# Optimization experiments

Hardware: AMD Instinct MI355X
Metric: run time of the kernel (lower is better)

Reference implementation:

```python
import jax, jax.numpy as jnp
import numpy as np

M, Q, H, L = 1, 9, 512, 2

def lstm_seq(x, w_ih, w_hh, b, reverse=False):
    # x: [B, T, Din] -> outputs [B, T, H], final (h, c) each [B, H]
    B = x.shape[0]
    h0 = jnp.zeros((B, H), x.dtype)
    xw = jnp.einsum('btd,gd->btg', x, w_ih) + b  # [B, T, 4H] input projection, precomputed
    def step(carry, xt):
        h, c = carry
        g = xt + h @ w_hh.T
        i, f, gg, o = jnp.split(g, 4, axis=-1)  # torch gate order: i, f, g, o
        c = jax.nn.sigmoid(f) * c + jax.nn.sigmoid(i) * jnp.tanh(gg)
        h = jax.nn.sigmoid(o) * jnp.tanh(c)
        return (h, c), h
    (hT, cT), hs = jax.lax.scan(step, (h0, h0), jnp.swapaxes(xw, 0, 1), reverse=reverse)
    return jnp.swapaxes(hs, 0, 1), hT, cT

def _forward(X, future_features, Y_teacher,
             enc_w_ih_l0, enc_w_hh_l0, enc_b_l0, enc_w_ih_l0r, enc_w_hh_l0r, enc_b_l0r,
             enc_w_ih_l1, enc_w_hh_l1, enc_b_l1, enc_w_ih_l1r, enc_w_hh_l1r, enc_b_l1r,
             dec_w_ih_l0, dec_w_hh_l0, dec_b_l0, dec_w_ih_l1, dec_w_hh_l1, dec_b_l1,
             bidi_w_h, bidi_b_h, out_w, out_b, horizon_span):
    B = X.shape[0]
    enc = [((enc_w_ih_l0, enc_w_hh_l0, enc_b_l0), (enc_w_ih_l0r, enc_w_hh_l0r, enc_b_l0r)),
           ((enc_w_ih_l1, enc_w_hh_l1, enc_b_l1), (enc_w_ih_l1r, enc_w_hh_l1r, enc_b_l1r))]
    inp, hs, cs = X, [], []
    for fw, bw in enc:  # bidirectional multilayer encoder
        of, hf, cf = lstm_seq(inp, *fw, reverse=False)
        ob, hb, cb = lstm_seq(inp, *bw, reverse=True)
        inp = jnp.concatenate([of, ob], axis=-1)
        hs += [hf, hb]; cs += [cf, cb]
    h = jnp.stack(hs)  # [2L, B, H], torch order (l0_fwd, l0_bwd, l1_fwd, l1_bwd)
    c = jnp.stack(cs)
    def merge(s):  # NOTE: original applies bidi_project__h / nonlin__h to BOTH h and c
        s = s.reshape(L, 2, B, H)
        s = jnp.concatenate([s[:, 0], s[:, 1]], axis=2)       # [L, B, 2H]
        s = jnp.swapaxes(s, 0, 1).reshape(B, 2 * L * H)
        s = jax.nn.elu(s @ bidi_w_h.T + bidi_b_h)             # [B, L*H]
        return jnp.swapaxes(s.reshape(B, L, H), 0, 1)         # [L, B, H]
    h, c = merge(h), merge(c)
    dec = [(dec_w_ih_l0, dec_w_hh_l0, dec_b_l0), (dec_w_ih_l1, dec_w_hh_l1, dec_b_l1)]
    def dec_step(carry, f_t):
        h, c, y_prev = carry
        x = jnp.concatenate([y_prev, f_t], axis=-1)  # [B, M + d_future_features]
        nh, nc = [], []
        for l, (w_ih, w_hh, b) in enumerate(dec):
            g = x @ w_ih.T + h[l] @ w_hh.T + b
            i, f, gg, o = jnp.split(g, 4, axis=-1)
            cl = jax.nn.sigmoid(f) * c[l] + jax.nn.sigmoid(i) * jnp.tanh(gg)
            x = jax.nn.sigmoid(o) * jnp.tanh(cl)
            nh.append(x); nc.append(cl)
        y = x @ out_w.T + out_b                       # [B, M*Q]
        return (jnp.stack(nh), jnp.stack(nc), y[:, :M]), y
    y0 = X[:, -1, :M]
    _, ys = jax.lax.scan(dec_step, (h, c, y0), jnp.swapaxes(future_features, 0, 1))
    T = future_features.shape[1]
    return jnp.swapaxes(ys, 0, 1).reshape(B, T, M, Q)

def setup_inputs() -> dict:
    key = jax.random.key(0)
    ks = iter(jax.random.split(key, 40))
    s = 0.05
    d = {
        'X': jax.random.normal(next(ks), (64, 256, 9), jnp.float32),
        'future_features': jax.random.normal(next(ks), (64, 96, 8), jnp.float32),
        'Y_teacher': jax.random.normal(next(ks), (64, 96, 1), jnp.float32),
    }
    shapes = {
        'enc_w_ih_l0': (2048, 9), 'enc_w_hh_l0': (2048, 512), 'enc_b_l0': (2048,),
        'enc_w_ih_l0r': (2048, 9), 'enc_w_hh_l0r': (2048, 512), 'enc_b_l0r': (2048,),
        'enc_w_ih_l1': (2048, 1024), 'enc_w_hh_l1': (2048, 512), 'enc_b_l1': (2048,),
        'enc_w_ih_l1r': (2048, 1024), 'enc_w_hh_l1r': (2048, 512), 'enc_b_l1r': (2048,),
        'dec_w_ih_l0': (2048, 9), 'dec_w_hh_l0': (2048, 512), 'dec_b_l0': (2048,),
        'dec_w_ih_l1': (2048, 512), 'dec_w_hh_l1': (2048, 512), 'dec_b_l1': (2048,),
        'bidi_w_h': (1024, 2048), 'bidi_b_h': (1024,),
        'out_w': (9, 512), 'out_b': (9,),
    }
    for name, shp in shapes.items():
        d[name] = jax.random.normal(next(ks), shp, jnp.float32) * s
    d['horizon_span'] = 96
    return d

def reference(X, future_features, Y_teacher,
              enc_w_ih_l0, enc_w_hh_l0, enc_b_l0, enc_w_ih_l0r, enc_w_hh_l0r, enc_b_l0r,
              enc_w_ih_l1, enc_w_hh_l1, enc_b_l1, enc_w_ih_l1r, enc_w_hh_l1r, enc_b_l1r,
              dec_w_ih_l0, dec_w_hh_l0, dec_b_l0, dec_w_ih_l1, dec_w_hh_l1, dec_b_l1,
              bidi_w_h, bidi_b_h, out_w, out_b, horizon_span):
    return _forward(X, future_features, Y_teacher,
                    enc_w_ih_l0, enc_w_hh_l0, enc_b_l0, enc_w_ih_l0r, enc_w_hh_l0r, enc_b_l0r,
                    enc_w_ih_l1, enc_w_hh_l1, enc_b_l1, enc_w_ih_l1r, enc_w_hh_l1r, enc_b_l1r,
                    dec_w_ih_l0, dec_w_hh_l0, dec_b_l0, dec_w_ih_l1, dec_w_hh_l1, dec_b_l1,
                    bidi_w_h, bidi_b_h, out_w, out_b, horizon_span)
```

## Files before the change

### kernel.cpp

```cpp
#include <hip/hip_runtime.h>


#define BLOCKS 256

typedef short bf16x8 __attribute__((ext_vector_type(8)));
typedef float f32x4  __attribute__((ext_vector_type(4)));
typedef unsigned short u16;

__device__ __forceinline__ f32x4 MFMA16(bf16x8 a, bf16x8 b, f32x4 c) {
  return __builtin_amdgcn_mfma_f32_16x16x32_bf16(a, b, c, 0, 0, 0);
}

__device__ __forceinline__ u16 bfr(float f) {
  unsigned u = __float_as_uint(f);
  u += 0x7FFFu + ((u >> 16) & 1u);
  return (u16)(u >> 16);
}
__device__ __forceinline__ bf16x8 pack8(float4 a, float4 b) {
  bf16x8 r;
  r[0] = (short)bfr(a.x); r[1] = (short)bfr(a.y); r[2] = (short)bfr(a.z); r[3] = (short)bfr(a.w);
  r[4] = (short)bfr(b.x); r[5] = (short)bfr(b.y); r[6] = (short)bfr(b.z); r[7] = (short)bfr(b.w);
  return r;
}
__device__ __forceinline__ bf16x8 loadW8(const float* p) {
  float4 a = *(const float4*)p;
  float4 b = *(const float4*)(p + 4);
  return pack8(a, b);
}
__device__ __forceinline__ float sigm(float x) { return 1.0f / (1.0f + __expf(-x)); }
__device__ __forceinline__ float tanh_f(float x) {
  float a = fabsf(x);
  float e = __expf(-2.0f * a);
  float t = (1.0f - e) / (1.0f + e);
  return x < 0.0f ? -t : t;
}
__device__ __forceinline__ float lstm_h(const float pre[4], float& c) {
  float ig = sigm(pre[0]);
  float fg = sigm(pre[1]);
  float gg = tanh_f(pre[2]);
  float og = sigm(pre[3]);
  c = fg * c + ig * gg;
  return og * tanh_f(c);
}

__device__ __forceinline__ void st_b16_coh(u16* p, u16 v) {
  unsigned uv = v;
  asm volatile("global_store_short %0, %1, off sc0 sc1" :: "v"(p), "v"(uv) : "memory");
}
__device__ __forceinline__ void st_f32_coh(float* p, float v) {
  asm volatile("global_store_dword %0, %1, off sc0 sc1" :: "v"(p), "v"(v) : "memory");
}
__device__ __forceinline__ void st_u32_coh(unsigned* p, unsigned v) {
  asm volatile("global_store_dword %0, %1, off sc0 sc1" :: "v"(p), "v"(v) : "memory");
}
__device__ __forceinline__ float ld_f32_coh(const float* p) {
  float r;
  asm volatile("global_load_dword %0, %1, off sc0 sc1\n\ts_waitcnt vmcnt(0)"
               : "=&v"(r) : "v"(p) : "memory");
  return r;
}
__device__ __forceinline__ unsigned ld_u32_coh(const unsigned* p) {
  unsigned r;
  asm volatile("global_load_dword %0, %1, off sc0 sc1\n\ts_waitcnt vmcnt(0)"
               : "=&v"(r) : "v"(p) : "memory");
  return r;
}
__device__ __forceinline__ void ld_tile_coh(const u16* base, bf16x8 f[16]) {
  asm volatile(
    "global_load_dwordx4 %0, %16, off sc0 sc1\n\t"
    "global_load_dwordx4 %1, %16, off offset:64 sc0 sc1\n\t"
    "global_load_dwordx4 %2, %16, off offset:128 sc0 sc1\n\t"
    "global_load_dwordx4 %3, %16, off offset:192 sc0 sc1\n\t"
    "global_load_dwordx4 %4, %16, off offset:256 sc0 sc1\n\t"
    "global_load_dwordx4 %5, %16, off offset:320 sc0 sc1\n\t"
    "global_load_dwordx4 %6, %16, off offset:384 sc0 sc1\n\t"
    "global_load_dwordx4 %7, %16, off offset:448 sc0 sc1\n\t"
    "global_load_dwordx4 %8, %16, off offset:512 sc0 sc1\n\t"
    "global_load_dwordx4 %9, %16, off offset:576 sc0 sc1\n\t"
    "global_load_dwordx4 %10, %16, off offset:640 sc0 sc1\n\t"
    "global_load_dwordx4 %11, %16, off offset:704 sc0 sc1\n\t"
    "global_load_dwordx4 %12, %16, off offset:768 sc0 sc1\n\t"
    "global_load_dwordx4 %13, %16, off offset:832 sc0 sc1\n\t"
    "global_load_dwordx4 %14, %16, off offset:896 sc0 sc1\n\t"
    "global_load_dwordx4 %15, %16, off offset:960 sc0 sc1\n\t"
    "s_waitcnt vmcnt(0)"
    : "=&v"(f[0]), "=&v"(f[1]), "=&v"(f[2]), "=&v"(f[3]),
      "=&v"(f[4]), "=&v"(f[5]), "=&v"(f[6]), "=&v"(f[7]),
      "=&v"(f[8]), "=&v"(f[9]), "=&v"(f[10]), "=&v"(f[11]),
      "=&v"(f[12]), "=&v"(f[13]), "=&v"(f[14]), "=&v"(f[15])
    : "v"(base)
    : "memory");
}

static constexpr size_t OFF_GO   = 32768;
static constexpr size_t OFF_YF   = 32896;
static constexpr size_t SZ_SLOT  = (size_t)64 * 512 * 2;
static constexpr size_t OFF_OF   = 65536;
static constexpr size_t OFF_OBR  = OFF_OF  + 257 * SZ_SLOT;
static constexpr size_t OFF_H1F  = OFF_OBR + 257 * SZ_SLOT;
static constexpr size_t OFF_H1B  = OFF_H1F + 2 * SZ_SLOT;
static constexpr size_t OFF_DH0  = OFF_H1B + 2 * SZ_SLOT;
static constexpr size_t OFF_DH1  = OFF_DH0 + 2 * SZ_SLOT;
static constexpr size_t OFF_SBUF = OFF_DH1 + 2 * SZ_SLOT;
static constexpr size_t OFF_CDEC = OFF_SBUF + (size_t)128 * 2048 * 4;
static constexpr size_t OFF_Y    = OFF_CDEC + (size_t)2 * 64 * 512 * 4;
static constexpr size_t WS_NEED  = OFF_Y + 256;

__device__ __forceinline__ void gridbar(char* ws, unsigned e) {
  asm volatile("s_waitcnt vmcnt(0)" ::: "memory");
  __syncthreads();
  unsigned* flags = (unsigned*)ws;
  unsigned* go    = (unsigned*)(ws + OFF_GO);
  const int tid = threadIdx.x;
  if (blockIdx.x == 0) {
    if (tid != 0) {
      const unsigned* fp = flags + (size_t)tid * 32;
      while (ld_u32_coh(fp) < e) {}
    }
    __syncthreads();
    if (tid == 0) st_u32_coh(go, e);
  } else {
    if (tid == 0) {
      st_u32_coh(flags + (size_t)blockIdx.x * 32, e);
      while (ld_u32_coh(go) < e) { __builtin_amdgcn_s_sleep(1); }
    }
    __syncthreads();
  }
}

__global__ __launch_bounds__(256, 1) void red_lstm(
    const float* __restrict__ X,   const float* __restrict__ FUT,
    const float* __restrict__ eWih0,  const float* __restrict__ eWhh0,  const float* __restrict__ eB0,
    const float* __restrict__ eWih0r, const float* __restrict__ eWhh0r, const float* __restrict__ eB0r,
    const float* __restrict__ eWih1,  const float* __restrict__ eWhh1,  const float* __restrict__ eB1,
    const float* __restrict__ eWih1r, const float* __restrict__ eWhh1r, const float* __restrict__ eB1r,
    const float* __restrict__ dWih0,  const float* __restrict__ dWhh0,  const float* __restrict__ dB0,
    const float* __restrict__ dWih1,  const float* __restrict__ dWhh1,  const float* __restrict__ dB1,
    const float* __restrict__ bW,  const float* __restrict__ bB,
    const float* __restrict__ oW,  const float* __restrict__ oB,
    float* __restrict__ OUT, char* __restrict__ ws)
{
  const int blk  = blockIdx.x;
  const int tid  = threadIdx.x;
  const int lane = tid & 63;
  const int wave = tid >> 6;
  const int n16  = lane & 15;
  const int quad = lane >> 4;
  const int rowg = wave * 16 + n16;
  const int jl   = tid & 3;
  const int bb   = tid >> 2;

  u16*   OF  = (u16*)(ws + OFF_OF);
  u16*   OBR = (u16*)(ws + OFF_OBR);
  u16*   H1F = (u16*)(ws + OFF_H1F);
  u16*   H1B = (u16*)(ws + OFF_H1B);
  u16*   DH0 = (u16*)(ws + OFF_DH0);
  u16*   DH1 = (u16*)(ws + OFF_DH1);
  float* SB  = (float*)(ws + OFF_SBUF);
  float* CD  = (float*)(ws + OFF_CDEC);
  float* YB  = (float*)(ws + OFF_Y);
  unsigned* YFLAG = (unsigned*)(ws + OFF_YF);

  __shared__ float g_s[64 * 20];
  unsigned ep = 0;

  {
    const bool fw = (blk < 128);
    const int  hb = fw ? blk : (blk - 128);
    const int  j0 = hb * 4;
    const int  col = j0 + (n16 & 3) + 512 * (n16 >> 2);
    const float* whh = fw ? eWhh0 : eWhh0r;
    const float* wih = fw ? eWih0 : eWih0r;
    const float* bia = fw ? eB0 : eB0r;
    u16* buf = fw ? OF : OBR;

    bf16x8 B[16];
    {
      const float* wr = whh + (size_t)col * 512 + quad * 8;
      #pragma unroll
      for (int kk = 0; kk < 16; ++kk) B[kk] = loadW8(wr + kk * 32);
    }
    float wr9[4][9], b4[4];
    #pragma unroll
    for (int g = 0; g < 4; ++g) {
      int cg = j0 + jl + 512 * g;
      b4[g] = bia[cg];
      #pragma unroll
      for (int k = 0; k < 9; ++k) wr9[g][k] = wih[cg * 9 + k];
    }
    float c = 0.0f;

    #pragma unroll 1
    for (int s = 0; s < 256; ++s) {
      bf16x8 T[16];
      ld_tile_coh(buf + ((size_t)s * 64 + rowg) * 512 + quad * 8, T);
      f32x4 a0 = {0.f,0.f,0.f,0.f}, a1 = {0.f,0.f,0.f,0.f};
      #pragma unroll
      for (int kk = 0; kk < 16; kk += 2) {
        a0 = MFMA16(T[kk],     B[kk],     a0);
        a1 = MFMA16(T[kk + 1], B[kk + 1], a1);
      }
      f32x4 acc = a0 + a1;
      #pragma unroll
      for (int r = 0; r < 4; ++r)
        g_s[(wave * 16 + quad * 4 + r) * 20 + n16] = acc[r];
      __syncthreads();

      const int t = fw ? s : (255 - s);
      float pre[4];
      #pragma unroll
      for (int g = 0; g < 4; ++g) pre[g] = g_s[bb * 20 + jl + 4 * g] + b4[g];
      const float* xp = X + ((size_t)bb * 256 + t) * 9;
      #pragma unroll
      for (int k = 0; k < 9; ++k) {
        float xv = xp[k];
        #pragma unroll
        for (int g = 0; g < 4; ++g) pre[g] += xv * wr9[g][k];
      }
      float h = lstm_h(pre, c);
      st_b16_coh(buf + ((size_t)(s + 1) * 64 + bb) * 512 + j0 + jl, bfr(h));
      if (s == 255) {
        int co = fw ? 0 : 512;
        st_f32_coh(SB + (size_t)bb * 2048 + co + j0 + jl, h);
        st_f32_coh(SB + (size_t)(64 + bb) * 2048 + co + j0 + jl, c);
      }
      gridbar(ws, ++ep);
    }
  }

  {
    const bool fw = (blk < 128);
    const int  hb = fw ? blk : (blk - 128);
    const int  j0 = hb * 4;
    const int  col = j0 + (n16 & 3) + 512 * (n16 >> 2);
    const float* whh = fw ? eWhh1 : eWhh1r;
    const float* wih = fw ? eWih1 : eWih1r;
    const float* bia = fw ? eB1 : eB1r;
    u16* hpp = fw ? H1F : H1B;

    bf16x8 B[48];
    {
      const float* wr = whh + (size_t)col * 512 + quad * 8;
      #pragma unroll
      for (int kk = 0; kk < 16; ++kk) B[kk] = loadW8(wr + kk * 32);
      const float* wr2 = wih + (size_t)col * 1024 + quad * 8;
      #pragma unroll
      for (int kk = 0; kk < 32; ++kk) B[16 + kk] = loadW8(wr2 + kk * 32);
    }
    float b4[4];
    #pragma unroll
    for (int g = 0; g < 4; ++g) b4[g] = bia[j0 + jl + 512 * g];
    float c = 0.0f;

    #pragma unroll 1
    for (int s = 0; s < 256; ++s) {
      const int slot_of = fw ? (s + 1)   : (256 - s);
      const int slot_ob = fw ? (256 - s) : (s + 1);
      f32x4 a0 = {0.f,0.f,0.f,0.f}, a1 = {0.f,0.f,0.f,0.f};
      {
        bf16x8 T[16];
        ld_tile_coh(hpp + ((size_t)(s & 1) * 64 + rowg) * 512 + quad * 8, T);
        #pragma unroll
        for (int kk = 0; kk < 16; kk += 2) {
          a0 = MFMA16(T[kk],     B[kk],     a0);
          a1 = MFMA16(T[kk + 1], B[kk + 1], a1);
        }
      }
      {
        bf16x8 T[16];
        ld_tile_coh(OF + ((size_t)slot_of * 64 + rowg) * 512 + quad * 8, T);
        #pragma unroll
        for (int kk = 0; kk < 16; kk += 2) {
          a0 = MFMA16(T[kk],     B[16 + kk],     a0);
          a1 = MFMA16(T[kk + 1], B[16 + kk + 1], a1);
        }
      }
      {
        bf16x8 T[16];
        ld_tile_coh(OBR + ((size_t)slot_ob * 64 + rowg) * 512 + quad * 8, T);
        #pragma unroll
        for (int kk = 0; kk < 16; kk += 2) {
          a0 = MFMA16(T[kk],     B[32 + kk],     a0);
          a1 = MFMA16(T[kk + 1], B[32 + kk + 1], a1);
        }
      }
      f32x4 acc = a0 + a1;
      #pragma unroll
      for (int r = 0; r < 4; ++r)
        g_s[(wave * 16 + quad * 4 + r) * 20 + n16] = acc[r];
      __syncthreads();

      float pre[4];
      #pragma unroll
      for (int g = 0; g < 4; ++g) pre[g] = g_s[bb * 20 + jl + 4 * g] + b4[g];
      float h = lstm_h(pre, c);
      st_b16_coh(hpp + ((size_t)((s & 1) ^ 1) * 64 + bb) * 512 + j0 + jl, bfr(h));
      if (s == 255) {
        int co = fw ? 1024 : 1536;
        st_f32_coh(SB + (size_t)bb * 2048 + co + j0 + jl, h);
        st_f32_coh(SB + (size_t)(64 + bb) * 2048 + co + j0 + jl, c);
      }
      gridbar(ws, ++ep);
    }
  }

  {
    if (blk < 128) {
      const int colm = blk * 8 + (tid & 7);
      const int rg   = tid >> 3;
      const float* wrow = bW + (size_t)colm * 2048;
      float am[4];
      #pragma unroll
      for (int r = 0; r < 4; ++r) am[r] = bB[colm];
      #pragma unroll 1
      for (int k = 0; k < 2048; k += 4) {
        float4 w = *(const float4*)(wrow + k);
        #pragma unroll
        for (int r = 0; r < 4; ++r) {
          float4 a = *(const float4*)(SB + (size_t)(rg * 4 + r) * 2048 + k);
          am[r] += a.x * w.x + a.y * w.y + a.z * w.z + a.w * w.w;
        }
      }
      const int l = colm >> 9, j = colm & 511;
      #pragma unroll
      for (int r = 0; r < 4; ++r) {
        int row = rg * 4 + r;
        float v = am[r];
        v = v > 0.f ? v : (__expf(v) - 1.0f);
        if (row < 64) {
          u16* dst = l ? DH1 : DH0;
          st_b16_coh(dst + (size_t)row * 512 + j, bfr(v));
        } else {
          st_f32_coh(CD + ((size_t)l * 64 + (row - 64)) * 512 + j, v);
        }
      }
    }
    gridbar(ws, ++ep);
  }

  {
    const bool isL0 = (blk < 128);
    const int  hb = isL0 ? blk : (blk - 128);
    const int  j0 = hb * 4;
    const int  col = j0 + (n16 & 3) + 512 * (n16 >> 2);

    bf16x8 BD[32];
    float wr9[4][9], b4[4], c;
    if (isL0) {
      const float* wr = dWhh0 + (size_t)col * 512 + quad * 8;
      #pragma unroll
      for (int kk = 0; kk < 16; ++kk) BD[kk] = loadW8(wr + kk * 32);
      #pragma unroll
      for (int g = 0; g < 4; ++g) {
        int cg = j0 + jl + 512 * g;
        b4[g] = dB0[cg];
        #pragma unroll
        for (int k = 0; k < 9; ++k) wr9[g][k] = dWih0[cg * 9 + k];
      }
      c = CD[(size_t)bb * 512 + j0 + jl];
    } else {
      const float* wr = dWhh1 + (size_t)col * 512 + quad * 8;
      #pragma unroll
      for (int kk = 0; kk < 16; ++kk) BD[kk] = loadW8(wr + kk * 32);
      const float* wr2 = dWih1 + (size_t)col * 512 + quad * 8;
      #pragma unroll
      for (int kk = 0; kk < 16; ++kk) BD[16 + kk] = loadW8(wr2 + kk * 32);
      #pragma unroll
      for (int g = 0; g < 4; ++g) b4[g] = dB1[j0 + jl + 512 * g];
      c = CD[((size_t)64 + bb) * 512 + j0 + jl];
    }
    bf16x8 OBW[16];
    float obv = 0.0f;
    if (blk == 128) {
      if (n16 < 9) {
        const float* wr = oW + (size_t)n16 * 512 + quad * 8;
        #pragma unroll
        for (int kk = 0; kk < 16; ++kk) OBW[kk] = loadW8(wr + kk * 32);
        obv = oB[n16];
      } else {
        #pragma unroll
        for (int kk = 0; kk < 16; ++kk) {
          bf16x8 z = {0,0,0,0,0,0,0,0};
          OBW[kk] = z;
        }
      }
    }

    #pragma unroll 1
    for (int t = 0; t < 96; ++t) {
      if (blk == 128 && t >= 1) {
        bf16x8 T[16];
        ld_tile_coh(DH1 + ((size_t)(t & 1) * 64 + rowg) * 512 + quad * 8, T);
        f32x4 a0 = {0.f,0.f,0.f,0.f}, a1 = {0.f,0.f,0.f,0.f};
        #pragma unroll
        for (int kk = 0; kk < 16; kk += 2) {
          a0 = MFMA16(T[kk],     OBW[kk],     a0);
          a1 = MFMA16(T[kk + 1], OBW[kk + 1], a1);
        }
        f32x4 acc = a0 + a1;
        #pragma unroll
        for (int r = 0; r < 4; ++r) {
          int b = wave * 16 + quad * 4 + r;
          float v = acc[r] + obv;
          if (n16 < 9) {
            OUT[(size_t)b * 864 + (size_t)(t - 1) * 9 + n16] = v;
            if (n16 == 0) st_f32_coh(YB + b, v);
          }
        }
        asm volatile("s_waitcnt vmcnt(0)" ::: "memory");
        __syncthreads();
        if (tid == 0) st_u32_coh(YFLAG, (unsigned)t);
      }
      if (isL0) {
        bf16x8 T[16];
        ld_tile_coh(DH0 + ((size_t)(t & 1) * 64 + rowg) * 512 + quad * 8, T);
        f32x4 a0 = {0.f,0.f,0.f,0.f}, a1 = {0.f,0.f,0.f,0.f};
        #pragma unroll
        for (int kk = 0; kk < 16; kk += 2) {
          a0 = MFMA16(T[kk],     BD[kk],     a0);
          a1 = MFMA16(T[kk + 1], BD[kk + 1], a1);
        }
        f32x4 acc = a0 + a1;
        #pragma unroll
        for (int r = 0; r < 4; ++r)
          g_s[(wave * 16 + quad * 4 + r) * 20 + n16] = acc[r];
        __syncthreads();
        if (t >= 1 && tid == 0) {
          while (ld_u32_coh(YFLAG) < (unsigned)t) {}
        }
        __syncthreads();
        float pre[4];
        #pragma unroll
        for (int g = 0; g < 4; ++g) pre[g] = g_s[bb * 20 + jl + 4 * g] + b4[g];
        float yp = (t == 0) ? X[((size_t)bb * 256 + 255) * 9] : ld_f32_coh(YB + bb);
        #pragma unroll
        for (int g = 0; g < 4; ++g) pre[g] += yp * wr9[g][0];
        const float* fp = FUT + ((size_t)bb * 96 + t) * 8;
        #pragma unroll
        for (int k = 0; k < 8; ++k) {
          float fv = fp[k];
          #pragma unroll
          for (int g = 0; g < 4; ++g) pre[g] += fv * wr9[g][k + 1];
        }
        float h = lstm_h(pre, c);
        st_b16_coh(DH0 + ((size_t)((t & 1) ^ 1) * 64 + bb) * 512 + j0 + jl, bfr(h));
      }
      gridbar(ws, ++ep);

      if (!isL0) {
        f32x4 a0 = {0.f,0.f,0.f,0.f}, a1 = {0.f,0.f,0.f,0.f};
        {
          bf16x8 T[16];
          ld_tile_coh(DH1 + ((size_t)(t & 1) * 64 + rowg) * 512 + quad * 8, T);
          #pragma unroll
          for (int kk = 0; kk < 16; kk += 2) {
            a0 = MFMA16(T[kk],     BD[kk],     a0);
            a1 = MFMA16(T[kk + 1], BD[kk + 1], a1);
          }
        }
        {
          bf16x8 T[16];
          ld_tile_coh(DH0 + ((size_t)((t & 1) ^ 1) * 64 + rowg) * 512 + quad * 8, T);
          #pragma unroll
          for (int kk = 0; kk < 16; kk += 2) {
            a0 = MFMA16(T[kk],     BD[16 + kk],     a0);
            a1 = MFMA16(T[kk + 1], BD[16 + kk + 1], a1);
          }
        }
        f32x4 acc = a0 + a1;
        #pragma unroll
        for (int r = 0; r < 4; ++r)
          g_s[(wave * 16 + quad * 4 + r) * 20 + n16] = acc[r];
        __syncthreads();
        float pre[4];
        #pragma unroll
        for (int g = 0; g < 4; ++g) pre[g] = g_s[bb * 20 + jl + 4 * g] + b4[g];
        float h = lstm_h(pre, c);
        st_b16_coh(DH1 + ((size_t)((t & 1) ^ 1) * 64 + bb) * 512 + j0 + jl, bfr(h));
      }
      gridbar(ws, ++ep);
    }

    if (blk == 128) {
      bf16x8 T[16];
      ld_tile_coh(DH1 + ((size_t)0 * 64 + rowg) * 512 + quad * 8, T);
      f32x4 a0 = {0.f,0.f,0.f,0.f}, a1 = {0.f,0.f,0.f,0.f};
      #pragma unroll
      for (int kk = 0; kk < 16; kk += 2) {
        a0 = MFMA16(T[kk],     OBW[kk],     a0);
        a1 = MFMA16(T[kk + 1], OBW[kk + 1], a1);
      }
      f32x4 acc = a0 + a1;
      #pragma unroll
      for (int r = 0; r < 4; ++r) {
        int b = wave * 16 + quad * 4 + r;
        float v = acc[r] + obv;
        if (n16 < 9) OUT[(size_t)b * 864 + (size_t)95 * 9 + n16] = v;
      }
    }
  }
}

extern "C" void kernel_launch(void* const* d_in, const int* in_sizes, int n_in,
                              void* d_out, int out_size, void* d_ws, size_t ws_size,
                              hipStream_t stream) {
  (void)in_sizes; (void)n_in; (void)out_size;
  if (ws_size < WS_NEED) return;

  const float* X      = (const float*)d_in[0];
  const float* FUT    = (const float*)d_in[1];
  const float* eWih0  = (const float*)d_in[3];
  const float* eWhh0  = (const float*)d_in[4];
  const float* eB0    = (const float*)d_in[5];
  const float* eWih0r = (const float*)d_in[6];
  const float* eWhh0r = (const float*)d_in[7];
  const float* eB0r   = (const float*)d_in[8];
  const float* eWih1  = (const float*)d_in[9];
  const float* eWhh1  = (const float*)d_in[10];
  const float* eB1    = (const float*)d_in[11];
  const float* eWih1r = (const float*)d_in[12];
  const float* eWhh1r = (const float*)d_in[13];
  const float* eB1r   = (const float*)d_in[14];
  const float* dWih0  = (const float*)d_in[15];
  const float* dWhh0  = (const float*)d_in[16];
  const float* dB0    = (const float*)d_in[17];
  const float* dWih1  = (const float*)d_in[18];
  const float* dWhh1  = (const float*)d_in[19];
  const float* dB1    = (const float*)d_in[20];
  const float* bW     = (const float*)d_in[21];
  const float* bB     = (const float*)d_in[22];
  const float* oW     = (const float*)d_in[23];
  const float* oB     = (const float*)d_in[24];

  char* ws = (char*)d_ws;
  hipMemsetAsync(ws, 0, 65536, stream);
  hipMemsetAsync(ws + OFF_OF, 0, SZ_SLOT, stream);
  hipMemsetAsync(ws + OFF_OBR, 0, SZ_SLOT, stream);
  hipMemsetAsync(ws + OFF_H1F, 0, SZ_SLOT, stream);
  hipMemsetAsync(ws + OFF_H1B, 0, SZ_SLOT, stream);

  red_lstm<<<BLOCKS, 256, 0, stream>>>(
      X, FUT,
      eWih0, eWhh0, eB0, eWih0r, eWhh0r, eB0r,
      eWih1, eWhh1, eB1, eWih1r, eWhh1r, eB1r,
      dWih0, dWhh0, dB0, dWih1, dWhh1, dB1,
      bW, bB, oW, oB,
      (float*)d_out, ws);
}
```

Measured before the change: 4.718 ms.

## Use write-once hidden-state slots with plain cached loads and per-block barrier flags

Hidden-state buffers for every recurrent stage become one slot per timestep instead of ping-pong double buffers. Because each address is now written only once, the A-operand tiles can be read with ordinary cached vector loads interleaved with the MFMAs, instead of coherent inline-asm loads that wait on the whole tile. The grid barrier gives each block its own go flag with no sleep, and the decoder's y feedback is published as per-block records, each with its own flag. This uses much more workspace and relies on stale cache lines never being read for fresh slots, which is a correctness risk if addresses are ever reused.

Result: slower. 6.376 ms (+35.2%).

```diff
diff --git a/kernel.cpp b/kernel.cpp
--- a/kernel.cpp
+++ b/kernel.cpp
@@ -50,14 +50,11 @@
 __device__ __forceinline__ void st_f32_coh(float* p, float v) {
   asm volatile("global_store_dword %0, %1, off sc0 sc1" :: "v"(p), "v"(v) : "memory");
 }
+__device__ __forceinline__ void st_f32x4_coh(float* p, f32x4 v) {
+  asm volatile("global_store_dwordx4 %0, %1, off sc0 sc1" :: "v"(p), "v"(v) : "memory");
+}
 __device__ __forceinline__ void st_u32_coh(unsigned* p, unsigned v) {
   asm volatile("global_store_dword %0, %1, off sc0 sc1" :: "v"(p), "v"(v) : "memory");
-}
-__device__ __forceinline__ float ld_f32_coh(const float* p) {
-  float r;
-  asm volatile("global_load_dword %0, %1, off sc0 sc1\n\ts_waitcnt vmcnt(0)"
-               : "=&v"(r) : "v"(p) : "memory");
-  return r;
 }
 __device__ __forceinline__ unsigned ld_u32_coh(const unsigned* p) {
   unsigned r;
@@ -65,51 +62,28 @@
                : "=&v"(r) : "v"(p) : "memory");
   return r;
 }
-__device__ __forceinline__ void ld_tile_coh(const u16* base, bf16x8 f[16]) {
-  asm volatile(
-    "global_load_dwordx4 %0, %16, off sc0 sc1\n\t"
-    "global_load_dwordx4 %1, %16, off offset:64 sc0 sc1\n\t"
-    "global_load_dwordx4 %2, %16, off offset:128 sc0 sc1\n\t"
-    "global_load_dwordx4 %3, %16, off offset:192 sc0 sc1\n\t"
-    "global_load_dwordx4 %4, %16, off offset:256 sc0 sc1\n\t"
-    "global_load_dwordx4 %5, %16, off offset:320 sc0 sc1\n\t"
-    "global_load_dwordx4 %6, %16, off offset:384 sc0 sc1\n\t"
-    "global_load_dwordx4 %7, %16, off offset:448 sc0 sc1\n\t"
-    "global_load_dwordx4 %8, %16, off offset:512 sc0 sc1\n\t"
-    "global_load_dwordx4 %9, %16, off offset:576 sc0 sc1\n\t"
-    "global_load_dwordx4 %10, %16, off offset:640 sc0 sc1\n\t"
-    "global_load_dwordx4 %11, %16, off offset:704 sc0 sc1\n\t"
-    "global_load_dwordx4 %12, %16, off offset:768 sc0 sc1\n\t"
-    "global_load_dwordx4 %13, %16, off offset:832 sc0 sc1\n\t"
-    "global_load_dwordx4 %14, %16, off offset:896 sc0 sc1\n\t"
-    "global_load_dwordx4 %15, %16, off offset:960 sc0 sc1\n\t"
-    "s_waitcnt vmcnt(0)"
-    : "=&v"(f[0]), "=&v"(f[1]), "=&v"(f[2]), "=&v"(f[3]),
-      "=&v"(f[4]), "=&v"(f[5]), "=&v"(f[6]), "=&v"(f[7]),
-      "=&v"(f[8]), "=&v"(f[9]), "=&v"(f[10]), "=&v"(f[11]),
-      "=&v"(f[12]), "=&v"(f[13]), "=&v"(f[14]), "=&v"(f[15])
-    : "v"(base)
-    : "memory");
-}
-
-static constexpr size_t OFF_GO   = 32768;
-static constexpr size_t OFF_YF   = 32896;
-static constexpr size_t SZ_SLOT  = (size_t)64 * 512 * 2;
-static constexpr size_t OFF_OF   = 65536;
-static constexpr size_t OFF_OBR  = OFF_OF  + 257 * SZ_SLOT;
-static constexpr size_t OFF_H1F  = OFF_OBR + 257 * SZ_SLOT;
-static constexpr size_t OFF_H1B  = OFF_H1F + 2 * SZ_SLOT;
-static constexpr size_t OFF_DH0  = OFF_H1B + 2 * SZ_SLOT;
-static constexpr size_t OFF_DH1  = OFF_DH0 + 2 * SZ_SLOT;
-static constexpr size_t OFF_SBUF = OFF_DH1 + 2 * SZ_SLOT;
-static constexpr size_t OFF_CDEC = OFF_SBUF + (size_t)128 * 2048 * 4;
-static constexpr size_t OFF_Y    = OFF_CDEC + (size_t)2 * 64 * 512 * 4;
-static constexpr size_t WS_NEED  = OFF_Y + 256;
+
+static constexpr size_t OFF_FLAGS = 0;
+static constexpr size_t OFF_GO    = 32768;
+static constexpr size_t SZ_YT     = (size_t)128 * 384;
+static constexpr size_t OFF_YREC  = 65536;
+static constexpr size_t OFF_SB    = OFF_YREC + 96 * SZ_YT;
+static constexpr size_t OFF_CD    = OFF_SB + (size_t)128 * 2048 * 4;
+static constexpr size_t SZ_SLOT   = (size_t)64 * 512 * 2;
+static constexpr size_t OFF_OF    = OFF_CD + (size_t)2 * 64 * 512 * 4;
+static constexpr size_t OFF_OBR   = OFF_OF  + 257 * SZ_SLOT;
+static constexpr size_t OFF_H1F   = OFF_OBR + 257 * SZ_SLOT;
+static constexpr size_t OFF_H1B   = OFF_H1F + 257 * SZ_SLOT;
+static constexpr size_t OFF_DH0   = OFF_H1B + 257 * SZ_SLOT;
+static constexpr size_t OFF_DH1   = OFF_DH0 + 97 * SZ_SLOT;
+static constexpr size_t WS_NEED   = OFF_DH1 + 97 * SZ_SLOT;
+
+#define SLOT_U 32768
 
 __device__ __forceinline__ void gridbar(char* ws, unsigned e) {
   asm volatile("s_waitcnt vmcnt(0)" ::: "memory");
   __syncthreads();
-  unsigned* flags = (unsigned*)ws;
+  unsigned* flags = (unsigned*)(ws + OFF_FLAGS);
   unsigned* go    = (unsigned*)(ws + OFF_GO);
   const int tid = threadIdx.x;
   if (blockIdx.x == 0) {
@@ -118,11 +92,12 @@
       while (ld_u32_coh(fp) < e) {}
     }
     __syncthreads();
-    if (tid == 0) st_u32_coh(go, e);
+    st_u32_coh(go + (size_t)tid * 32, e);
   } else {
     if (tid == 0) {
       st_u32_coh(flags + (size_t)blockIdx.x * 32, e);
-      while (ld_u32_coh(go) < e) { __builtin_amdgcn_s_sleep(1); }
+      const unsigned* gp = go + (size_t)blockIdx.x * 32;
+      while (ld_u32_coh(gp) < e) {}
     }
     __syncthreads();
   }
@@ -156,12 +131,11 @@
   u16*   H1B = (u16*)(ws + OFF_H1B);
   u16*   DH0 = (u16*)(ws + OFF_DH0);
   u16*   DH1 = (u16*)(ws + OFF_DH1);
-  float* SB  = (float*)(ws + OFF_SBUF);
-  float* CD  = (float*)(ws + OFF_CDEC);
-  float* YB  = (float*)(ws + OFF_Y);
-  unsigned* YFLAG = (unsigned*)(ws + OFF_YF);
+  float* SB  = (float*)(ws + OFF_SB);
+  float* CD  = (float*)(ws + OFF_CD);
 
   __shared__ float g_s[64 * 20];
+  __shared__ __align__(16) float y_s[64];
   unsigned ep = 0;
 
   {
@@ -192,13 +166,12 @@
 
     #pragma unroll 1
     for (int s = 0; s < 256; ++s) {
-      bf16x8 T[16];
-      ld_tile_coh(buf + ((size_t)s * 64 + rowg) * 512 + quad * 8, T);
+      const u16* ab = buf + (size_t)s * SLOT_U + rowg * 512 + quad * 8;
       f32x4 a0 = {0.f,0.f,0.f,0.f}, a1 = {0.f,0.f,0.f,0.f};
       #pragma unroll
       for (int kk = 0; kk < 16; kk += 2) {
-        a0 = MFMA16(T[kk],     B[kk],     a0);
-        a1 = MFMA16(T[kk + 1], B[kk + 1], a1);
+        a0 = MFMA16(*(const bf16x8*)(ab + kk * 32),        B[kk],     a0);
+        a1 = MFMA16(*(const bf16x8*)(ab + kk * 32 + 32),   B[kk + 1], a1);
       }
       f32x4 acc = a0 + a1;
       #pragma unroll
@@ -218,7 +191,7 @@
         for (int g = 0; g < 4; ++g) pre[g] += xv * wr9[g][k];
       }
       float h = lstm_h(pre, c);
-      st_b16_coh(buf + ((size_t)(s + 1) * 64 + bb) * 512 + j0 + jl, bfr(h));
+      st_b16_coh(buf + (size_t)(s + 1) * SLOT_U + bb * 512 + j0 + jl, bfr(h));
       if (s == 255) {
         int co = fw ? 0 : 512;
         st_f32_coh(SB + (size_t)bb * 2048 + co + j0 + jl, h);
@@ -256,33 +229,24 @@
     for (int s = 0; s < 256; ++s) {
       const int slot_of = fw ? (s + 1)   : (256 - s);
       const int slot_ob = fw ? (256 - s) : (s + 1);
+      const u16* aH = hpp + (size_t)s * SLOT_U + rowg * 512 + quad * 8;
+      const u16* aF = OF  + (size_t)slot_of * SLOT_U + rowg * 512 + quad * 8;
+      const u16* aB = OBR + (size_t)slot_ob * SLOT_U + rowg * 512 + quad * 8;
       f32x4 a0 = {0.f,0.f,0.f,0.f}, a1 = {0.f,0.f,0.f,0.f};
-      {
-        bf16x8 T[16];
-        ld_tile_coh(hpp + ((size_t)(s & 1) * 64 + rowg) * 512 + quad * 8, T);
-        #pragma unroll
-        for (int kk = 0; kk < 16; kk += 2) {
-          a0 = MFMA16(T[kk],     B[kk],     a0);
-          a1 = MFMA16(T[kk + 1], B[kk + 1], a1);
-        }
-      }
-      {
-        bf16x8 T[16];
-        ld_tile_coh(OF + ((size_t)slot_of * 64 + rowg) * 512 + quad * 8, T);
-        #pragma unroll
-        for (int kk = 0; kk < 16; kk += 2) {
-          a0 = MFMA16(T[kk],     B[16 + kk],     a0);
-          a1 = MFMA16(T[kk + 1], B[16 + kk + 1], a1);
-        }
-      }
-      {
-        bf16x8 T[16];
-        ld_tile_coh(OBR + ((size_t)slot_ob * 64 + rowg) * 512 + quad * 8, T);
-        #pragma unroll
-        for (int kk = 0; kk < 16; kk += 2) {
-          a0 = MFMA16(T[kk],     B[32 + kk],     a0);
-          a1 = MFMA16(T[kk + 1], B[32 + kk + 1], a1);
-        }
+      #pragma unroll
+      for (int kk = 0; kk < 16; kk += 2) {
+        a0 = MFMA16(*(const bf16x8*)(aH + kk * 32),      B[kk],     a0);
+        a1 = MFMA16(*(const bf16x8*)(aH + kk * 32 + 32), B[kk + 1], a1);
+      }
+      #pragma unroll
+      for (int kk = 0; kk < 16; kk += 2) {
+        a0 = MFMA16(*(const bf16x8*)(aF + kk * 32),      B[16 + kk],     a0);
+        a1 = MFMA16(*(const bf16x8*)(aF + kk * 32 + 32), B[16 + kk + 1], a1);
+      }
+      #pragma unroll
+      for (int kk = 0; kk < 16; kk += 2) {
+        a0 = MFMA16(*(const bf16x8*)(aB + kk * 32),      B[32 + kk],     a0);
+        a1 = MFMA16(*(const bf16x8*)(aB + kk * 32 + 32), B[32 + kk + 1], a1);
       }
       f32x4 acc = a0 + a1;
       #pragma unroll
@@ -294,7 +258,7 @@
       #pragma unroll
       for (int g = 0; g < 4; ++g) pre[g] = g_s[bb * 20 + jl + 4 * g] + b4[g];
       float h = lstm_h(pre, c);
-      st_b16_coh(hpp + ((size_t)((s & 1) ^ 1) * 64 + bb) * 512 + j0 + jl, bfr(h));
+      st_b16_coh(hpp + (size_t)(s + 1) * SLOT_U + bb * 512 + j0 + jl, bfr(h));
       if (s == 255) {
         int co = fw ? 1024 : 1536;
         st_f32_coh(SB + (size_t)bb * 2048 + co + j0 + jl, h);
@@ -389,52 +353,55 @@
     #pragma unroll 1
     for (int t = 0; t < 96; ++t) {
       if (blk == 128 && t >= 1) {
-        bf16x8 T[16];
-        ld_tile_coh(DH1 + ((size_t)(t & 1) * 64 + rowg) * 512 + quad * 8, T);
+        const u16* ah = DH1 + (size_t)t * SLOT_U + rowg * 512 + quad * 8;
         f32x4 a0 = {0.f,0.f,0.f,0.f}, a1 = {0.f,0.f,0.f,0.f};
         #pragma unroll
         for (int kk = 0; kk < 16; kk += 2) {
-          a0 = MFMA16(T[kk],     OBW[kk],     a0);
-          a1 = MFMA16(T[kk + 1], OBW[kk + 1], a1);
+          a0 = MFMA16(*(const bf16x8*)(ah + kk * 32),      OBW[kk],     a0);
+          a1 = MFMA16(*(const bf16x8*)(ah + kk * 32 + 32), OBW[kk + 1], a1);
         }
         f32x4 acc = a0 + a1;
         #pragma unroll
         for (int r = 0; r < 4; ++r) {
           int b = wave * 16 + quad * 4 + r;
           float v = acc[r] + obv;
-          if (n16 < 9) {
-            OUT[(size_t)b * 864 + (size_t)(t - 1) * 9 + n16] = v;
-            if (n16 == 0) st_f32_coh(YB + b, v);
+          if (n16 < 9) OUT[(size_t)b * 864 + (size_t)(t - 1) * 9 + n16] = v;
+          if (n16 == 0) y_s[b] = v;
+        }
+        __syncthreads();
+        {
+          char* yt = ws + OFF_YREC + (size_t)t * SZ_YT;
+          const int rec = tid >> 1, half = tid & 1;
+          float* dst = (float*)(yt + (size_t)rec * 384) + half * 32;
+          #pragma unroll
+          for (int i = 0; i < 8; ++i) {
+            f32x4 v = *(const f32x4*)(y_s + half * 32 + i * 4);
+            st_f32x4_coh(dst + i * 4, v);
           }
         }
         asm volatile("s_waitcnt vmcnt(0)" ::: "memory");
         __syncthreads();
-        if (tid == 0) st_u32_coh(YFLAG, (unsigned)t);
+        if (tid < 128) {
+          unsigned* yf = (unsigned*)(ws + OFF_YREC + (size_t)t * SZ_YT + (size_t)tid * 384 + 256);
+          st_u32_coh(yf, (unsigned)t);
+        }
       }
       if (isL0) {
-        bf16x8 T[16];
-        ld_tile_coh(DH0 + ((size_t)(t & 1) * 64 + rowg) * 512 + quad * 8, T);
+        const u16* ah = DH0 + (size_t)t * SLOT_U + rowg * 512 + quad * 8;
         f32x4 a0 = {0.f,0.f,0.f,0.f}, a1 = {0.f,0.f,0.f,0.f};
         #pragma unroll
         for (int kk = 0; kk < 16; kk += 2) {
-          a0 = MFMA16(T[kk],     BD[kk],     a0);
-          a1 = MFMA16(T[kk + 1], BD[kk + 1], a1);
+          a0 = MFMA16(*(const bf16x8*)(ah + kk * 32),      BD[kk],     a0);
+          a1 = MFMA16(*(const bf16x8*)(ah + kk * 32 + 32), BD[kk + 1], a1);
         }
         f32x4 acc = a0 + a1;
         #pragma unroll
         for (int r = 0; r < 4; ++r)
           g_s[(wave * 16 + quad * 4 + r) * 20 + n16] = acc[r];
         __syncthreads();
-        if (t >= 1 && tid == 0) {
-          while (ld_u32_coh(YFLAG) < (unsigned)t) {}
-        }
-        __syncthreads();
         float pre[4];
         #pragma unroll
         for (int g = 0; g < 4; ++g) pre[g] = g_s[bb * 20 + jl + 4 * g] + b4[g];
-        float yp = (t == 0) ? X[((size_t)bb * 256 + 255) * 9] : ld_f32_coh(YB + bb);
-        #pragma unroll
-        for (int g = 0; g < 4; ++g) pre[g] += yp * wr9[g][0];
         const float* fp = FUT + ((size_t)bb * 96 + t) * 8;
         #pragma unroll
         for (int k = 0; k < 8; ++k) {
@@ -442,30 +409,37 @@
           #pragma unroll
           for (int g = 0; g < 4; ++g) pre[g] += fv * wr9[g][k + 1];
         }
+        float yp;
+        if (t == 0) {
+          yp = X[((size_t)bb * 256 + 255) * 9];
+        } else {
+          char* yr = ws + OFF_YREC + (size_t)t * SZ_YT + (size_t)blk * 384;
+          if (tid == 0) {
+            while (ld_u32_coh((unsigned*)(yr + 256)) < (unsigned)t) {}
+          }
+          __syncthreads();
+          yp = ((const float*)yr)[bb];
+        }
+        #pragma unroll
+        for (int g = 0; g < 4; ++g) pre[g] += yp * wr9[g][0];
         float h = lstm_h(pre, c);
-        st_b16_coh(DH0 + ((size_t)((t & 1) ^ 1) * 64 + bb) * 512 + j0 + jl, bfr(h));
+        st_b16_coh(DH0 + (size_t)(t + 1) * SLOT_U + bb * 512 + j0 + jl, bfr(h));
       }
       gridbar(ws, ++ep);
 
       if (!isL0) {
+        const u16* ah = DH1 + (size_t)t * SLOT_U + rowg * 512 + quad * 8;
+        const u16* ax = DH0 + (size_t)(t + 1) * SLOT_U + rowg * 512 + quad * 8;
         f32x4 a0 = {0.f,0.f,0.f,0.f}, a1 = {0.f,0.f,0.f,0.f};
-        {
-          bf16x8 T[16];
-          ld_tile_coh(DH1 + ((size_t)(t & 1) * 64 + rowg) * 512 + quad * 8, T);
-          #pragma unroll
-          for (int kk = 0; kk < 16; kk += 2) {
-            a0 = MFMA16(T[kk],     BD[kk],     a0);
-            a1 = MFMA16(T[kk + 1], BD[kk + 1], a1);
-          }
-        }
-        {
-          bf16x8 T[16];
-          ld_tile_coh(DH0 + ((size_t)((t & 1) ^ 1) * 64 + rowg) * 512 + quad * 8, T);
-          #pragma unroll
-          for (int kk = 0; kk < 16; kk += 2) {
-            a0 = MFMA16(T[kk],     BD[16 + kk],     a0);
-            a1 = MFMA16(T[kk + 1], BD[16 + kk + 1], a1);
-          }
+        #pragma unroll
+        for (int kk = 0; kk < 16; kk += 2) {
+          a0 = MFMA16(*(const bf16x8*)(ah + kk * 32),      BD[kk],     a0);
+          a1 = MFMA16(*(const bf16x8*)(ah + kk * 32 + 32), BD[kk + 1], a1);
+        }
+        #pragma unroll
+        for (int kk = 0; kk < 16; kk += 2) {
+          a0 = MFMA16(*(const bf16x8*)(ax + kk * 32),      BD[16 + kk],     a0);
+          a1 = MFMA16(*(const bf16x8*)(ax + kk * 32 + 32), BD[16 + kk + 1], a1);
         }
         f32x4 acc = a0 + a1;
         #pragma unroll
@@ -476,19 +450,18 @@
         #pragma unroll
         for (int g = 0; g < 4; ++g) pre[g] = g_s[bb * 20 + jl + 4 * g] + b4[g];
         float h = lstm_h(pre, c);
-        st_b16_coh(DH1 + ((size_t)((t & 1) ^ 1) * 64 + bb) * 512 + j0 + jl, bfr(h));
+        st_b16_coh(DH1 + (size_t)(t + 1) * SLOT_U + bb * 512 + j0 + jl, bfr(h));
       }
       gridbar(ws, ++ep);
     }
 
     if (blk == 128) {
-      bf16x8 T[16];
-      ld_tile_coh(DH1 + ((size_t)0 * 64 + rowg) * 512 + quad * 8, T);
+      const u16* ah = DH1 + (size_t)96 * SLOT_U + rowg * 512 + quad * 8;
       f32x4 a0 = {0.f,0.f,0.f,0.f}, a1 = {0.f,0.f,0.f,0.f};
       #pragma unroll
       for (int kk = 0; kk < 16; kk += 2) {
-        a0 = MFMA16(T[kk],     OBW[kk],     a0);
-        a1 = MFMA16(T[kk + 1], OBW[kk + 1], a1);
+        a0 = MFMA16(*(const bf16x8*)(ah + kk * 32),      OBW[kk],     a0);
+        a1 = MFMA16(*(const bf16x8*)(ah + kk * 32 + 32), OBW[kk + 1], a1);
       }
       f32x4 acc = a0 + a1;
       #pragma unroll
@@ -533,8 +506,8 @@
   const float* oB     = (const float*)d_in[24];
 
   char* ws = (char*)d_ws;
-  hipMemsetAsync(ws, 0, 65536, stream);
-  hipMemsetAsync(ws + OFF_OF, 0, SZ_SLOT, stream);
+  hipMemsetAsync(ws, 0, OFF_SB, stream);
+  hipMemsetAsync(ws + OFF_OF,  0, SZ_SLOT, stream);
   hipMemsetAsync(ws + OFF_OBR, 0, SZ_SLOT, stream);
   hipMemsetAsync(ws + OFF_H1F, 0, SZ_SLOT, stream);
   hipMemsetAsync(ws + OFF_H1B, 0, SZ_SLOT, stream);
```
